# Performance work log

Measured on AMD Instinct MI355X. Metric: run time of the kernel, lower is better.

The kernel has to match this reference:

```python
import jax, jax.numpy as jnp
import numpy as np


def _embedding_distances(dictionary, x_flat):
    # dictionary: [D, C], x_flat: [T, C] -> [T, D]
    dict_norms = jnp.sum(dictionary * dictionary, axis=-1)          # [D]
    x_norms = jnp.sum(x_flat * x_flat, axis=-1)                     # [T]
    dots = jnp.einsum('tc,dc->td', x_flat, dictionary)              # [T, D]
    return -2.0 * dots + dict_norms[None, :] + x_norms[:, None]


def _quantize(x, dictionary):
    # x: [N, C, H, W]
    N, C, H, W = x.shape
    cl = jnp.transpose(x, (0, 2, 3, 1))                             # [N, H, W, C]
    diffs = _embedding_distances(dictionary, cl.reshape(-1, C))     # [NHW, D]
    idxs = jnp.argmin(diffs, axis=-1).reshape(N, H, W)              # [N, H, W]
    embedded = jnp.transpose(dictionary[idxs], (0, 3, 1, 2))        # [N, C, H, W]
    embedded_pt = jax.lax.stop_gradient(embedded) + (x - jax.lax.stop_gradient(x))
    return embedded, embedded_pt, idxs


def setup_inputs() -> dict:
    key = jax.random.key(0)
    k1, k2, k3 = jax.random.split(key, 3)
    N, C, H, W, D = 32, 256, 32, 32, 1024
    return {
        'inputs': jax.random.normal(k1, (N, C, H, W), dtype=jnp.float32),
        'inputs_thermal': jax.random.normal(k2, (N, C, H, W), dtype=jnp.float32),
        'dictionary': jax.random.normal(k3, (D, C), dtype=jnp.float32),
    }


def reference(inputs, inputs_thermal, dictionary):
    embedded, embedded_pt, idxs = _quantize(inputs, dictionary)
    embedded_t, embedded_pt_t, idxs_t = _quantize(inputs_thermal, dictionary)
    return (embedded, embedded_pt, idxs, embedded_t, embedded_pt_t, idxs_t)
```

## Files before the change

### kernel.cpp

```cpp
#include <hip/hip_runtime.h>

#define NB    32
#define CCH   256
#define HW    1024
#define NPIX  (NB*HW)
#define DDICT 1024

#define EMB_ELEMS  ((size_t)NB*CCH*HW)
#define SEC_ELEMS  (2*EMB_ELEMS + NPIX)

#define TPX  256
#define TD   128
#define NDT  (DDICT/TD)
#define BK   32
#define NKC  (CCH/BK)
#define NPH  (NDT*NKC)

#define TAU  0.05f

#define RPX  16

typedef __attribute__((ext_vector_type(8))) short bf16x8;
typedef __attribute__((ext_vector_type(4))) float f32x4;

__device__ inline ushort split_rne(float f, float& rest) {
    uint u = __float_as_uint(f);
    uint r = u + 0x7FFFu + ((u >> 16) & 1u);
    rest = f - __uint_as_float(r & 0xFFFF0000u);
    return (ushort)(r >> 16);
}

__device__ inline ushort rne_bf16(float f) {
    uint u = __float_as_uint(f);
    return (ushort)((u + 0x7FFFu + ((u >> 16) & 1u)) >> 16);
}

__device__ inline void gll16(const void* g, void* l) {
    __builtin_amdgcn_global_load_lds(
        (const __attribute__((address_space(1))) uint*)g,
        (__attribute__((address_space(3))) uint*)l,
        16, 0, 0);
}

__device__ inline void nts16(float* p, float a, float b, float c, float d) {
    f32x4 v = {a, b, c, d};
    __builtin_nontemporal_store(v, (f32x4*)p);
}

__global__ void dict_norms_kernel(const float* __restrict__ dict,
                                  float* __restrict__ norms,
                                  int* __restrict__ cnts) {
    if (blockIdx.x == 0 && threadIdx.x < 2) cnts[threadIdx.x] = 0;
    int d = blockIdx.x * blockDim.x + threadIdx.x;
    if (d < DDICT) {
        const float4* row = (const float4*)(dict + (size_t)d * CCH);
        float s = 0.f;
#pragma unroll 8
        for (int i = 0; i < CCH / 4; ++i) {
            float4 v = row[i];
            s += v.x * v.x + v.y * v.y + v.z * v.z + v.w * v.w;
        }
        norms[d] = s;
    }
}

__global__ void dict_split_kernel(const float* __restrict__ dict,
                                  ushort* __restrict__ dHs,
                                  ushort* __restrict__ dMs,
                                  float* __restrict__ dictT) {
    int d = blockIdx.x;
    int lane = threadIdx.x;
    float4 f = ((const float4*)(dict + (size_t)d * CCH))[lane];
    float v[4] = {f.x, f.y, f.z, f.w};
    ushort h[4], m[4];
#pragma unroll
    for (int i = 0; i < 4; ++i) {
        float r1;
        h[i] = split_rne(v[i], r1);
        m[i] = rne_bf16(r1);
    }
    int c0 = lane * 4;
    int kc = c0 >> 5, oct = (c0 >> 3) & 3, e0 = c0 & 7;
    int dt = d >> 7, dd = d & 127;
    int slot = (oct + (dd >> 1)) & 3;
    size_t base = ((size_t)(dt * NKC + kc)) * 4096 + dd * 32 + slot * 8 + e0;
    *(ushort4*)(dHs + base) = make_ushort4(h[0], h[1], h[2], h[3]);
    *(ushort4*)(dMs + base) = make_ushort4(m[0], m[1], m[2], m[3]);
#pragma unroll
    for (int j = 0; j < 4; ++j)
        dictT[(size_t)(c0 + j) * DDICT + d] = v[j];
}

__global__ __launch_bounds__(512, 1)
void vq_mfma_kernel(const float* __restrict__ x0,
                    const float* __restrict__ x1,
                    const ushort* __restrict__ dHs,
                    const ushort* __restrict__ dMs,
                    const float* __restrict__ norms,
                    const float* __restrict__ dict,
                    float* __restrict__ out,
                    int* __restrict__ cnts,
                    int* __restrict__ lists) {
    __shared__ ushort Bs[2][2][4096];
    __shared__ float nrm_s[DDICT];
    __shared__ int   idx_s[TPX];

    const int t    = threadIdx.x;
    const int lane = t & 63;
    const int wv   = t >> 6;
    const int lx   = lane & 15;
    const int q    = lane >> 4;
    const int m0w  = wv * 32;
    const int z    = blockIdx.y;

    const int g0  = blockIdx.x * TPX;
    const int n   = g0 / HW;
    const int hw0 = g0 % HW;

    const float* x = z ? x1 : x0;
    float* out_base = out + (size_t)z * SEC_ELEMS;
    float* out_idx  = out_base + 2 * EMB_ELEMS;
    int* cnt  = cnts + z;
    int* list = lists + (size_t)z * NPIX;

    *(float2*)(nrm_s + t * 2) = *(const float2*)(norms + t * 2);

    const float* xbase = x + (size_t)n * CCH * HW + hw0 + m0w + lx;
    bf16x8 Ah[8][2], Am[8][2];
#pragma unroll
    for (int kc = 0; kc < NKC; ++kc) {
        float a_f[2][8];
#pragma unroll
        for (int mi = 0; mi < 2; ++mi)
#pragma unroll
            for (int j = 0; j < 8; ++j)
                a_f[mi][j] = xbase[(size_t)(kc * BK + q * 8 + j) * HW + mi * 16];
#pragma unroll
        for (int mi = 0; mi < 2; ++mi)
#pragma unroll
            for (int j = 0; j < 8; ++j) {
                float r1;
                ushort h = split_rne(a_f[mi][j], r1);
                Ah[kc][mi][j] = (short)h;
                Am[kc][mi][j] = (short)rne_bf16(r1);
            }
    }

    auto stage = [&](int p, int b) {
#pragma unroll
        for (int plane = 0; plane < 2; ++plane) {
            const ushort* sp = (plane ? dMs : dHs) + (size_t)p * 4096;
            gll16(sp + t * 8, &Bs[b][plane][wv * 512]);
        }
    };

    __syncthreads();
    stage(0, 0);

    float b1r[2][4], b2r[2][4]; int i1r[2][4];
#pragma unroll
    for (int mi = 0; mi < 2; ++mi)
#pragma unroll
        for (int r = 0; r < 4; ++r) {
            b1r[mi][r] = 3.0e38f; b2r[mi][r] = 3.0e38f; i1r[mi][r] = 0;
        }

    for (int dt = 0; dt < NDT; ++dt) {
        f32x4 acc[2][8] = {};
#pragma unroll
        for (int kc = 0; kc < NKC; ++kc) {
            const int p = dt * 8 + kc;
            asm volatile("s_waitcnt vmcnt(0)" ::: "memory");
            __builtin_amdgcn_s_barrier();
            if (p + 1 < NPH) stage(p + 1, (p + 1) & 1);

            const ushort* bb = &Bs[p & 1][0][0];
            __builtin_amdgcn_s_setprio(1);
#pragma unroll
            for (int ni = 0; ni < 8; ++ni) {
                int nn   = ni * 16 + lx;
                int slot = (q + (nn >> 1)) & 3;
                int off  = nn * 32 + slot * 8;
                bf16x8 Bh = *(const bf16x8*)(bb + off);
                bf16x8 Bm = *(const bf16x8*)(bb + 4096 + off);
#pragma unroll
                for (int mi = 0; mi < 2; ++mi) {
                    f32x4 c = acc[mi][ni];
                    c = __builtin_amdgcn_mfma_f32_16x16x32_bf16(Ah[kc][mi], Bh, c, 0, 0, 0);
                    c = __builtin_amdgcn_mfma_f32_16x16x32_bf16(Ah[kc][mi], Bm, c, 0, 0, 0);
                    c = __builtin_amdgcn_mfma_f32_16x16x32_bf16(Am[kc][mi], Bh, c, 0, 0, 0);
                    acc[mi][ni] = c;
                }
            }
            __builtin_amdgcn_s_setprio(0);
        }

        const int d0 = dt * TD;
        float nrm[8];
#pragma unroll
        for (int ni = 0; ni < 8; ++ni) nrm[ni] = nrm_s[d0 + ni * 16 + lx];

#pragma unroll
        for (int mi = 0; mi < 2; ++mi)
#pragma unroll
            for (int r = 0; r < 4; ++r) {
                float c1 = 3.0e38f, c2 = 3.0e38f; int ci = 0;
#pragma unroll
                for (int ni = 0; ni < 8; ++ni) {
                    float dist = fmaf(-2.f, acc[mi][ni][r], nrm[ni]);
                    if (dist < c1)      { c2 = c1; c1 = dist; ci = ni * 16 + lx; }
                    else if (dist < c2) { c2 = dist; }
                }
#pragma unroll
                for (int off = 1; off < 16; off <<= 1) {
                    float o1 = __shfl_xor(c1, off);
                    int   oi = __shfl_xor(ci, off);
                    float o2 = __shfl_xor(c2, off);
                    if (o1 < c1 || (o1 == c1 && oi < ci)) {
                        c2 = fminf(c1, o2); c1 = o1; ci = oi;
                    } else {
                        c2 = fminf(c2, o1);
                    }
                }
                if (c1 < b1r[mi][r]) {
                    b2r[mi][r] = fminf(b1r[mi][r], c2);
                    b1r[mi][r] = c1;
                    i1r[mi][r] = d0 + ci;
                } else {
                    b2r[mi][r] = fminf(b2r[mi][r], c1);
                }
            }
    }

#pragma unroll
    for (int mi = 0; mi < 2; ++mi)
#pragma unroll
        for (int r = 0; r < 4; ++r) {
            if (lx == 0) {
                int loc = m0w + mi * 16 + q * 4 + r;
                int g = g0 + loc;
                idx_s[loc] = i1r[mi][r];
                out_idx[g] = (float)i1r[mi][r];
                if (b2r[mi][r] - b1r[mi][r] < TAU) {
                    int slot = atomicAdd(cnt, 1);
                    list[slot] = g;
                }
            }
        }
    __syncthreads();

    const int pg = t & 63;
    const int cg = t >> 6;
    const int hwp = hw0 + pg * 4;
    const float* r0 = dict + (size_t)idx_s[pg * 4 + 0] * CCH;
    const float* r1 = dict + (size_t)idx_s[pg * 4 + 1] * CCH;
    const float* r2 = dict + (size_t)idx_s[pg * 4 + 2] * CCH;
    const float* r3 = dict + (size_t)idx_s[pg * 4 + 3] * CCH;
    float* oe = out_base;
    float* op = out_base + EMB_ELEMS;
    const size_t obase = (size_t)n * CCH * HW + hwp;

#pragma unroll
    for (int cq = 0; cq < 8; ++cq) {
        int c = cg * 32 + cq * 4;
        float4 q0 = *(const float4*)(r0 + c);
        float4 q1 = *(const float4*)(r1 + c);
        float4 q2 = *(const float4*)(r2 + c);
        float4 q3 = *(const float4*)(r3 + c);
        nts16(oe + obase + (size_t)(c + 0) * HW, q0.x, q1.x, q2.x, q3.x);
        nts16(op + obase + (size_t)(c + 0) * HW, q0.x, q1.x, q2.x, q3.x);
        nts16(oe + obase + (size_t)(c + 1) * HW, q0.y, q1.y, q2.y, q3.y);
        nts16(op + obase + (size_t)(c + 1) * HW, q0.y, q1.y, q2.y, q3.y);
        nts16(oe + obase + (size_t)(c + 2) * HW, q0.z, q1.z, q2.z, q3.z);
        nts16(op + obase + (size_t)(c + 2) * HW, q0.z, q1.z, q2.z, q3.z);
        nts16(oe + obase + (size_t)(c + 3) * HW, q0.w, q1.w, q2.w, q3.w);
        nts16(op + obase + (size_t)(c + 3) * HW, q0.w, q1.w, q2.w, q3.w);
    }
}

__global__ __launch_bounds__(256)
void vq_rescue_kernel(const float* __restrict__ x0,
                      const float* __restrict__ x1,
                      const float* __restrict__ dictT,
                      const float* __restrict__ dict,
                      const float* __restrict__ norms,
                      const int* __restrict__ cnts,
                      const int* __restrict__ lists,
                      float* __restrict__ out) {
    __shared__ float xr[CCH][RPX];
    __shared__ float rd_s[4][RPX];
    __shared__ int   ri_s[4][RPX];
    __shared__ int   gi_s[RPX];
    __shared__ int   bi_s[RPX];
    const int z = blockIdx.y;
    const float* x = z ? x1 : x0;
    const int* list = lists + (size_t)z * NPIX;
    float* out_emb    = out + (size_t)z * SEC_ELEMS;
    float* out_emb_pt = out_emb + EMB_ELEMS;
    float* out_idx    = out_emb + 2 * EMB_ELEMS;
    const int t    = threadIdx.x;
    const int lane = t & 63;
    const int wv   = t >> 6;
    const int total = cnts[z];

    for (int w0 = blockIdx.x * RPX; w0 < total; w0 += gridDim.x * RPX) {
        const int np = min(RPX, total - w0);
        if (t < RPX) gi_s[t] = list[w0 + ((t < np) ? t : (np - 1))];
        __syncthreads();

        {
            const int p  = t >> 4;
            const int j0 = (t & 15) * 16;
            const int g  = gi_s[p];
            const int n  = g / HW, hw = g % HW;
            const float* xb = x + (size_t)n * CCH * HW + hw;
#pragma unroll
            for (int j = 0; j < 16; ++j)
                xr[j0 + j][p] = xb[(size_t)(j0 + j) * HW];
        }
        __syncthreads();

        float acc[4][RPX] = {};
        for (int k = 0; k < CCH; ++k) {
            float xp[RPX];
#pragma unroll
            for (int p4 = 0; p4 < RPX / 4; ++p4) {
                f32x4 v = *(const f32x4*)&xr[k][p4 * 4];
#pragma unroll
                for (int j = 0; j < 4; ++j) xp[p4 * 4 + j] = v[j];
            }
#pragma unroll
            for (int dd = 0; dd < 4; ++dd) {
                float v = dictT[(size_t)k * DDICT + dd * 256 + t];
#pragma unroll
                for (int p = 0; p < RPX; ++p)
                    acc[dd][p] = fmaf(xp[p], v, acc[dd][p]);
            }
        }

#pragma unroll
        for (int p = 0; p < RPX; ++p) {
            float bd = 3.0e38f; int bi = 0;
#pragma unroll
            for (int dd = 0; dd < 4; ++dd) {
                int d = dd * 256 + t;
                float dist = fmaf(-2.f, acc[dd][p], norms[d]);
                if (dist < bd) { bd = dist; bi = d; }
            }
#pragma unroll
            for (int off = 1; off < 64; off <<= 1) {
                float od = __shfl_xor(bd, off);
                int   oi = __shfl_xor(bi, off);
                if (od < bd || (od == bd && oi < bi)) { bd = od; bi = oi; }
            }
            if (lane == 0) { rd_s[wv][p] = bd; ri_s[wv][p] = bi; }
        }
        __syncthreads();
        if (t < RPX) {
            const int p = t;
            float fb = rd_s[0][p]; int fi = ri_s[0][p];
#pragma unroll
            for (int q2 = 1; q2 < 4; ++q2)
                if (rd_s[q2][p] < fb || (rd_s[q2][p] == fb && ri_s[q2][p] < fi)) {
                    fb = rd_s[q2][p]; fi = ri_s[q2][p];
                }
            bi_s[p] = fi;
            if (p < np) out_idx[gi_s[p]] = (float)fi;
        }
        __syncthreads();

        {
            const int p  = t >> 4;
            const int j0 = (t & 15) * 16;
            if (p < np) {
                const int g = gi_s[p];
                const int n = g / HW, hw = g % HW;
                const float* dr = dict + (size_t)bi_s[p] * CCH;
                const size_t ob = (size_t)n * CCH * HW + hw;
#pragma unroll
                for (int j = 0; j < 16; ++j) {
                    float v = dr[j0 + j];
                    out_emb[ob + (size_t)(j0 + j) * HW]    = v;
                    out_emb_pt[ob + (size_t)(j0 + j) * HW] = v;
                }
            }
        }
        __syncthreads();
    }
}

extern "C" void kernel_launch(void* const* d_in, const int* in_sizes, int n_in,
                              void* d_out, int out_size, void* d_ws, size_t ws_size,
                              hipStream_t stream) {
    const float* x0   = (const float*)d_in[0];
    const float* x1   = (const float*)d_in[1];
    const float* dict = (const float*)d_in[2];
    float* out = (float*)d_out;

    float*  norms = (float*)d_ws;
    ushort* dHs   = (ushort*)(norms + DDICT);
    ushort* dMs   = dHs + (size_t)DDICT * CCH;
    float*  dictT = (float*)(dMs + (size_t)DDICT * CCH);
    int*    lists = (int*)(dictT + (size_t)DDICT * CCH);
    int*    cnts  = lists + 2 * NPIX;

    dict_norms_kernel<<<dim3(DDICT / 256), dim3(256), 0, stream>>>(dict, norms, cnts);
    dict_split_kernel<<<dim3(DDICT), dim3(64), 0, stream>>>(dict, dHs, dMs, dictT);

    vq_mfma_kernel<<<dim3(NPIX / TPX, 2), dim3(512), 0, stream>>>(
        x0, x1, dHs, dMs, norms, dict, out, cnts, lists);

    vq_rescue_kernel<<<dim3(512, 2), dim3(256), 0, stream>>>(
        x0, x1, dictT, dict, norms, cnts, lists, out);
}
```

Measured before the change: 421.0 us.

## Halve pixel tile per block to raise occupancy and use plain stores

Each block now covers 128 pixels instead of 256, and each wave owns one 16-row MFMA tile instead of two. This cuts A-fragment and accumulator registers so launch bounds can allow up to 4 blocks per CU, which doubles the grid and gives more waves to hide latency. The cost is that every LDS B fragment now feeds half as many MFMAs, and dictionary staging traffic across blocks doubles. The embedding write-out also switches from nontemporal stores to ordinary float4 stores.

```diff
diff --git a/kernel.cpp b/kernel.cpp
--- a/kernel.cpp
+++ b/kernel.cpp
@@ -9,7 +9,7 @@
 #define EMB_ELEMS  ((size_t)NB*CCH*HW)
 #define SEC_ELEMS  (2*EMB_ELEMS + NPIX)
 
-#define TPX  256
+#define TPX  128
 #define TD   128
 #define NDT  (DDICT/TD)
 #define BK   32
@@ -40,11 +40,6 @@
         (const __attribute__((address_space(1))) uint*)g,
         (__attribute__((address_space(3))) uint*)l,
         16, 0, 0);
-}
-
-__device__ inline void nts16(float* p, float a, float b, float c, float d) {
-    f32x4 v = {a, b, c, d};
-    __builtin_nontemporal_store(v, (f32x4*)p);
 }
 
 __global__ void dict_norms_kernel(const float* __restrict__ dict,
@@ -91,7 +86,7 @@
         dictT[(size_t)(c0 + j) * DDICT + d] = v[j];
 }
 
-__global__ __launch_bounds__(512, 1)
+__global__ __launch_bounds__(512, 4)
 void vq_mfma_kernel(const float* __restrict__ x0,
                     const float* __restrict__ x1,
                     const ushort* __restrict__ dHs,
@@ -110,7 +105,7 @@
     const int wv   = t >> 6;
     const int lx   = lane & 15;
     const int q    = lane >> 4;
-    const int m0w  = wv * 32;
+    const int m0w  = wv * 16;
     const int z    = blockIdx.y;
 
     const int g0  = blockIdx.x * TPX;
@@ -126,24 +121,20 @@
     *(float2*)(nrm_s + t * 2) = *(const float2*)(norms + t * 2);
 
     const float* xbase = x + (size_t)n * CCH * HW + hw0 + m0w + lx;
-    bf16x8 Ah[8][2], Am[8][2];
+    bf16x8 Ah[8], Am[8];
 #pragma unroll
     for (int kc = 0; kc < NKC; ++kc) {
-        float a_f[2][8];
-#pragma unroll
-        for (int mi = 0; mi < 2; ++mi)
-#pragma unroll
-            for (int j = 0; j < 8; ++j)
-                a_f[mi][j] = xbase[(size_t)(kc * BK + q * 8 + j) * HW + mi * 16];
-#pragma unroll
-        for (int mi = 0; mi < 2; ++mi)
-#pragma unroll
-            for (int j = 0; j < 8; ++j) {
-                float r1;
-                ushort h = split_rne(a_f[mi][j], r1);
-                Ah[kc][mi][j] = (short)h;
-                Am[kc][mi][j] = (short)rne_bf16(r1);
-            }
+        float a_f[8];
+#pragma unroll
+        for (int j = 0; j < 8; ++j)
+            a_f[j] = xbase[(size_t)(kc * BK + q * 8 + j) * HW];
+#pragma unroll
+        for (int j = 0; j < 8; ++j) {
+            float r1;
+            ushort h = split_rne(a_f[j], r1);
+            Ah[kc][j] = (short)h;
+            Am[kc][j] = (short)rne_bf16(r1);
+        }
     }
 
     auto stage = [&](int p, int b) {
@@ -157,16 +148,14 @@
     __syncthreads();
     stage(0, 0);
 
-    float b1r[2][4], b2r[2][4]; int i1r[2][4];
-#pragma unroll
-    for (int mi = 0; mi < 2; ++mi)
-#pragma unroll
-        for (int r = 0; r < 4; ++r) {
-            b1r[mi][r] = 3.0e38f; b2r[mi][r] = 3.0e38f; i1r[mi][r] = 0;
-        }
+    float b1r[4], b2r[4]; int i1r[4];
+#pragma unroll
+    for (int r = 0; r < 4; ++r) {
+        b1r[r] = 3.0e38f; b2r[r] = 3.0e38f; i1r[r] = 0;
+    }
 
     for (int dt = 0; dt < NDT; ++dt) {
-        f32x4 acc[2][8] = {};
+        f32x4 acc[8] = {};
 #pragma unroll
         for (int kc = 0; kc < NKC; ++kc) {
             const int p = dt * 8 + kc;
@@ -183,14 +172,11 @@
                 int off  = nn * 32 + slot * 8;
                 bf16x8 Bh = *(const bf16x8*)(bb + off);
                 bf16x8 Bm = *(const bf16x8*)(bb + 4096 + off);
-#pragma unroll
-                for (int mi = 0; mi < 2; ++mi) {
-                    f32x4 c = acc[mi][ni];
-                    c = __builtin_amdgcn_mfma_f32_16x16x32_bf16(Ah[kc][mi], Bh, c, 0, 0, 0);
-                    c = __builtin_amdgcn_mfma_f32_16x16x32_bf16(Ah[kc][mi], Bm, c, 0, 0, 0);
-                    c = __builtin_amdgcn_mfma_f32_16x16x32_bf16(Am[kc][mi], Bh, c, 0, 0, 0);
-                    acc[mi][ni] = c;
-                }
+                f32x4 c = acc[ni];
+                c = __builtin_amdgcn_mfma_f32_16x16x32_bf16(Ah[kc], Bh, c, 0, 0, 0);
+                c = __builtin_amdgcn_mfma_f32_16x16x32_bf16(Ah[kc], Bm, c, 0, 0, 0);
+                c = __builtin_amdgcn_mfma_f32_16x16x32_bf16(Am[kc], Bh, c, 0, 0, 0);
+                acc[ni] = c;
             }
             __builtin_amdgcn_s_setprio(0);
         }
@@ -201,56 +187,52 @@
         for (int ni = 0; ni < 8; ++ni) nrm[ni] = nrm_s[d0 + ni * 16 + lx];
 
 #pragma unroll
-        for (int mi = 0; mi < 2; ++mi)
-#pragma unroll
-            for (int r = 0; r < 4; ++r) {
-                float c1 = 3.0e38f, c2 = 3.0e38f; int ci = 0;
-#pragma unroll
-                for (int ni = 0; ni < 8; ++ni) {
-                    float dist = fmaf(-2.f, acc[mi][ni][r], nrm[ni]);
-                    if (dist < c1)      { c2 = c1; c1 = dist; ci = ni * 16 + lx; }
-                    else if (dist < c2) { c2 = dist; }
+        for (int r = 0; r < 4; ++r) {
+            float c1 = 3.0e38f, c2 = 3.0e38f; int ci = 0;
+#pragma unroll
+            for (int ni = 0; ni < 8; ++ni) {
+                float dist = fmaf(-2.f, acc[ni][r], nrm[ni]);
+                if (dist < c1)      { c2 = c1; c1 = dist; ci = ni * 16 + lx; }
+                else if (dist < c2) { c2 = dist; }
+            }
+#pragma unroll
+            for (int off = 1; off < 16; off <<= 1) {
+                float o1 = __shfl_xor(c1, off);
+                int   oi = __shfl_xor(ci, off);
+                float o2 = __shfl_xor(c2, off);
+                if (o1 < c1 || (o1 == c1 && oi < ci)) {
+                    c2 = fminf(c1, o2); c1 = o1; ci = oi;
+                } else {
+                    c2 = fminf(c2, o1);
                 }
-#pragma unroll
-                for (int off = 1; off < 16; off <<= 1) {
-                    float o1 = __shfl_xor(c1, off);
-                    int   oi = __shfl_xor(ci, off);
-                    float o2 = __shfl_xor(c2, off);
-                    if (o1 < c1 || (o1 == c1 && oi < ci)) {
-                        c2 = fminf(c1, o2); c1 = o1; ci = oi;
-                    } else {
-                        c2 = fminf(c2, o1);
-                    }
-                }
-                if (c1 < b1r[mi][r]) {
-                    b2r[mi][r] = fminf(b1r[mi][r], c2);
-                    b1r[mi][r] = c1;
-                    i1r[mi][r] = d0 + ci;
-                } else {
-                    b2r[mi][r] = fminf(b2r[mi][r], c1);
-                }
-            }
-    }
-
-#pragma unroll
-    for (int mi = 0; mi < 2; ++mi)
-#pragma unroll
-        for (int r = 0; r < 4; ++r) {
-            if (lx == 0) {
-                int loc = m0w + mi * 16 + q * 4 + r;
-                int g = g0 + loc;
-                idx_s[loc] = i1r[mi][r];
-                out_idx[g] = (float)i1r[mi][r];
-                if (b2r[mi][r] - b1r[mi][r] < TAU) {
-                    int slot = atomicAdd(cnt, 1);
-                    list[slot] = g;
-                }
-            }
-        }
+            }
+            if (c1 < b1r[r]) {
+                b2r[r] = fminf(b1r[r], c2);
+                b1r[r] = c1;
+                i1r[r] = d0 + ci;
+            } else {
+                b2r[r] = fminf(b2r[r], c1);
+            }
+        }
+    }
+
+#pragma unroll
+    for (int r = 0; r < 4; ++r) {
+        if (lx == 0) {
+            int loc = m0w + q * 4 + r;
+            int g = g0 + loc;
+            idx_s[loc] = i1r[r];
+            out_idx[g] = (float)i1r[r];
+            if (b2r[r] - b1r[r] < TAU) {
+                int slot = atomicAdd(cnt, 1);
+                list[slot] = g;
+            }
+        }
+    }
     __syncthreads();
 
-    const int pg = t & 63;
-    const int cg = t >> 6;
+    const int pg = t & 31;
+    const int cg = t >> 5;
     const int hwp = hw0 + pg * 4;
     const float* r0 = dict + (size_t)idx_s[pg * 4 + 0] * CCH;
     const float* r1 = dict + (size_t)idx_s[pg * 4 + 1] * CCH;
@@ -261,20 +243,24 @@
     const size_t obase = (size_t)n * CCH * HW + hwp;
 
 #pragma unroll
-    for (int cq = 0; cq < 8; ++cq) {
-        int c = cg * 32 + cq * 4;
+    for (int cq = 0; cq < 4; ++cq) {
+        int c = cg * 16 + cq * 4;
         float4 q0 = *(const float4*)(r0 + c);
         float4 q1 = *(const float4*)(r1 + c);
         float4 q2 = *(const float4*)(r2 + c);
         float4 q3 = *(const float4*)(r3 + c);
-        nts16(oe + obase + (size_t)(c + 0) * HW, q0.x, q1.x, q2.x, q3.x);
-        nts16(op + obase + (size_t)(c + 0) * HW, q0.x, q1.x, q2.x, q3.x);
-        nts16(oe + obase + (size_t)(c + 1) * HW, q0.y, q1.y, q2.y, q3.y);
-        nts16(op + obase + (size_t)(c + 1) * HW, q0.y, q1.y, q2.y, q3.y);
-        nts16(oe + obase + (size_t)(c + 2) * HW, q0.z, q1.z, q2.z, q3.z);
-        nts16(op + obase + (size_t)(c + 2) * HW, q0.z, q1.z, q2.z, q3.z);
-        nts16(oe + obase + (size_t)(c + 3) * HW, q0.w, q1.w, q2.w, q3.w);
-        nts16(op + obase + (size_t)(c + 3) * HW, q0.w, q1.w, q2.w, q3.w);
+        float4 v0 = make_float4(q0.x, q1.x, q2.x, q3.x);
+        float4 v1 = make_float4(q0.y, q1.y, q2.y, q3.y);
+        float4 v2 = make_float4(q0.z, q1.z, q2.z, q3.z);
+        float4 v3 = make_float4(q0.w, q1.w, q2.w, q3.w);
+        *(float4*)(oe + obase + (size_t)(c + 0) * HW) = v0;
+        *(float4*)(op + obase + (size_t)(c + 0) * HW) = v0;
+        *(float4*)(oe + obase + (size_t)(c + 1) * HW) = v1;
+        *(float4*)(op + obase + (size_t)(c + 1) * HW) = v1;
+        *(float4*)(oe + obase + (size_t)(c + 2) * HW) = v2;
+        *(float4*)(op + obase + (size_t)(c + 2) * HW) = v2;
+        *(float4*)(oe + obase + (size_t)(c + 3) * HW) = v3;
+        *(float4*)(op + obase + (size_t)(c + 3) * HW) = v3;
     }
 }
 
```

Result: faster. 393.6 us (-6.5%).
